# Optimization experiments

Hardware: AMD Instinct MI355X
Metric: run time of the kernel (lower is better)

## Reference

```python
import jax, jax.numpy as jnp
import numpy as np

DIM = 768
HEADS = 12
HEAD_DIM = DIM // HEADS
SCALE = DIM ** (-0.5)  # NOTE: module scales by full dim, not head_dim


def setup_inputs() -> dict:
    key = jax.random.key(0)
    k1, k2, k3 = jax.random.split(key, 3)
    B, N = 4, 2048
    x = jax.random.normal(k1, (B, N, DIM), dtype=jnp.float32)
    W_qkv = jax.random.normal(k2, (DIM, 3 * DIM), dtype=jnp.float32) * (DIM ** -0.5)
    W_proj = jax.random.normal(k3, (DIM, DIM), dtype=jnp.float32) * (DIM ** -0.5)
    b_proj = jnp.zeros((DIM,), dtype=jnp.float32)
    return {"x": x, "W_qkv": W_qkv, "W_proj": W_proj, "b_proj": b_proj}


def reference(x, W_qkv, W_proj, b_proj):
    B, N, C = x.shape
    qkv = x @ W_qkv  # [B, N, 3C]
    qkv = qkv.reshape(B, N, 3, HEADS, HEAD_DIM)
    qkv = jnp.transpose(qkv, (2, 0, 3, 1, 4))  # [3, B, H, N, hd]
    q, k, v = qkv[0], qkv[1], qkv[2]
    att = jnp.einsum('bhnd,bhmd->bhnm', q, k) * SCALE
    att = jax.nn.softmax(att, axis=-1)
    # drop=0.0 -> dropout is identity
    out = jnp.einsum('bhnm,bhmd->bhnd', att, v)  # [B, H, N, hd]
    out = jnp.transpose(out, (0, 2, 1, 3)).reshape(B, N, C)
    return out @ W_proj + b_proj
```

## Files before the change

kernel.cpp:

```cpp
#include <hip/hip_runtime.h>
#include <hip/hip_bf16.h>

#define HEADS 12
#define HD    64
#define SEQ   2048
#define CDIM  768
#define QKV_SCALE 0.03608439182435161f
#define LOG2E 1.4426950408889634f
#define SM_C (QKV_SCALE * LOG2E)

typedef __attribute__((ext_vector_type(8))) short bf16x8;
typedef __attribute__((ext_vector_type(4))) float f32x4;
typedef __attribute__((ext_vector_type(4))) unsigned short usx4;
typedef __attribute__((ext_vector_type(8))) unsigned short usx8;
typedef __attribute__((ext_vector_type(2))) unsigned int uix2;
typedef __attribute__((ext_vector_type(4))) unsigned int uix4;

__device__ __forceinline__ unsigned short f2bf(float f) {
  union { __hip_bfloat16 h; unsigned short u; } c;
  c.h = __float2bfloat16(f);
  return c.u;
}

__device__ __forceinline__ float exp2_fast(float x) {
  float r; asm("v_exp_f32 %0, %1" : "=v"(r) : "v"(x)); return r;
}

__device__ __forceinline__ unsigned int cvt_pk_bf16(float lo, float hi) {
  unsigned int r; asm("v_cvt_pk_bf16_f32 %0, %1, %2" : "=v"(r) : "v"(lo), "v"(hi)); return r;
}

__device__ __forceinline__ void gload_lds16(const unsigned short* g, unsigned short* l) {
  __builtin_amdgcn_global_load_lds(
      (__attribute__((address_space(1))) void*)(g),
      (__attribute__((address_space(3))) void*)(l), 16, 0, 0);
}

__global__ __launch_bounds__(256) void k_cvt_x(const float* __restrict__ src,
                                               unsigned short* __restrict__ dst) {
  int i = blockIdx.x * 256 + threadIdx.x;
  const float4* s4 = (const float4*)src;
  float4 a = s4[i * 2 + 0];
  float4 b = s4[i * 2 + 1];
  usx8 r;
  r[0] = f2bf(a.x); r[1] = f2bf(a.y); r[2] = f2bf(a.z); r[3] = f2bf(a.w);
  r[4] = f2bf(b.x); r[5] = f2bf(b.y); r[6] = f2bf(b.z); r[7] = f2bf(b.w);
  *(usx8*)&dst[i * 8] = r;
}

__global__ __launch_bounds__(256) void k_transpose(const float* __restrict__ src,
                                                   unsigned short* __restrict__ dst,
                                                   int K, int C) {
  __shared__ float tile[32][33];
  int tx = threadIdx.x & 31;
  int ty = threadIdx.x >> 5;
  int c0 = blockIdx.x * 32;
  int k0 = blockIdx.y * 32;
#pragma unroll
  for (int i = 0; i < 32; i += 8)
    tile[ty + i][tx] = src[(size_t)(k0 + ty + i) * C + c0 + tx];
  __syncthreads();
#pragma unroll
  for (int i = 0; i < 32; i += 8)
    dst[(size_t)(c0 + ty + i) * K + k0 + tx] = f2bf(tile[tx][ty + i]);
}

__global__ __launch_bounds__(256) void k_qkv_gemm(
    const unsigned short* __restrict__ A,
    const unsigned short* __restrict__ Bt,
    unsigned short* __restrict__ Qb, unsigned short* __restrict__ Kb,
    unsigned short* __restrict__ Vt) {
  __shared__ unsigned short As[128 * 64];
  __shared__ unsigned short Bs[128 * 64];
  const int lane = threadIdx.x & 63, w = threadIdx.x >> 6;
  const int wm = w >> 1, wn = w & 1;
  const int r0 = blockIdx.y * 128, c0 = blockIdx.x * 128;
  f32x4 acc[4][4] = {};

  for (int k0 = 0; k0 < 768; k0 += 64) {
#pragma unroll
    for (int iss = 0; iss < 4; ++iss) {
      int eo = (w * 4 + iss) * 512 + lane * 8;
      int row = eo >> 6;
      int cc = ((eo >> 3) & 7) ^ (row & 7);
      gload_lds16(A + (size_t)(r0 + row) * 768 + k0 + cc * 8, &As[(w * 4 + iss) * 512]);
    }
#pragma unroll
    for (int iss = 0; iss < 4; ++iss) {
      int eo = (w * 4 + iss) * 512 + lane * 8;
      int row = eo >> 6;
      int cc = ((eo >> 3) & 7) ^ (row & 7);
      gload_lds16(Bt + (size_t)(c0 + row) * 768 + k0 + cc * 8, &Bs[(w * 4 + iss) * 512]);
    }
    asm volatile("s_waitcnt vmcnt(0)" ::: "memory");
    __syncthreads();

#pragma unroll
    for (int ks = 0; ks < 2; ++ks) {
      bf16x8 af[4], bfr[4];
#pragma unroll
      for (int f = 0; f < 4; ++f) {
        int ar = wm * 64 + f * 16 + (lane & 15);
        int ac = (ks * 4 + (lane >> 4)) ^ (ar & 7);
        af[f] = *(const bf16x8*)&As[ar * 64 + ac * 8];
        int br = wn * 64 + f * 16 + (lane & 15);
        int bc = (ks * 4 + (lane >> 4)) ^ (br & 7);
        bfr[f] = *(const bf16x8*)&Bs[br * 64 + bc * 8];
      }
#pragma unroll
      for (int fm = 0; fm < 4; ++fm)
#pragma unroll
        for (int fn = 0; fn < 4; ++fn)
          acc[fm][fn] = __builtin_amdgcn_mfma_f32_16x16x32_bf16(af[fm], bfr[fn], acc[fm][fn], 0, 0, 0);
    }
    __syncthreads();
  }

  const int which = c0 / 768;
  const float qsc = (which == 0) ? SM_C : 1.0f;
#pragma unroll
  for (int fm = 0; fm < 4; ++fm) {
    int gr0 = r0 + wm * 64 + fm * 16 + ((lane >> 4) << 2);
    int bb = gr0 >> 11, n0 = gr0 & 2047;
#pragma unroll
    for (int fn = 0; fn < 4; ++fn) {
      int gc = c0 + wn * 64 + fn * 16 + (lane & 15);
      int rem = gc - which * 768;
      int h = rem >> 6, d = rem & 63;
      int bh = bb * HEADS + h;
      f32x4 v = acc[fm][fn];
      if (which == 2) {
        usx4 p;
        p[0] = f2bf(v[0]); p[1] = f2bf(v[1]); p[2] = f2bf(v[2]); p[3] = f2bf(v[3]);
        *(usx4*)&Vt[(size_t)(bh * 64 + d) * 2048 + n0] = p;
      } else {
        unsigned short* dst = (which == 0 ? Qb : Kb) + (size_t)(bh * 2048 + n0) * 64 + d;
        dst[0]   = f2bf(v[0] * qsc);
        dst[64]  = f2bf(v[1] * qsc);
        dst[128] = f2bf(v[2] * qsc);
        dst[192] = f2bf(v[3] * qsc);
      }
    }
  }
}

__global__ __launch_bounds__(256, 2) void k_attn(
    const unsigned short* __restrict__ Qb, const unsigned short* __restrict__ Kb,
    const unsigned short* __restrict__ Vt, unsigned short* __restrict__ Ob) {
  __shared__ unsigned short Ksm[2][64 * 64];
  __shared__ unsigned short Vsm[2][64 * 64];
  const int lane = threadIdx.x & 63, w = threadIdx.x >> 6;
  const int g = lane >> 4, c = lane & 15;

  int id = blockIdx.x + (blockIdx.y << 4);
  int lin = (id & 7) * 96 + (id >> 3);
  int bx = lin & 15, bh = lin >> 4;
  const int q0 = bx * 128 + w * 32;
  const int bb = bh / HEADS, h = bh % HEADS;

  const unsigned short* Qp = Qb + (size_t)bh * SEQ * HD;
  const unsigned short* Kp = Kb + (size_t)bh * SEQ * HD;
  const unsigned short* Vp = Vt + (size_t)bh * HD * SEQ;

  bf16x8 aQ[2][2];
#pragma unroll
  for (int qf = 0; qf < 2; ++qf)
#pragma unroll
    for (int ks = 0; ks < 2; ++ks)
      aQ[qf][ks] = *(const bf16x8*)&Qp[(size_t)(q0 + qf * 16 + c) * 64 + ks * 32 + g * 8];

  float lrun[2] = {0.f, 0.f};
  f32x4 accOT[4][2] = {};
  const f32x4 fzero = {0.f, 0.f, 0.f, 0.f};

  int offf[2][4];
#pragma unroll
  for (int ks = 0; ks < 2; ++ks)
#pragma unroll
    for (int f = 0; f < 4; ++f) {
      int row = f * 16 + c;
      offf[ks][f] = row * 64 + (((ks * 4 + g) ^ (row & 7)) * 8);
    }

  const int eo0 = (w * 2 + 0) * 512 + lane * 8;
  const int row0 = eo0 >> 6, cc0 = ((eo0 >> 3) & 7) ^ (row0 & 7);
  const int eo1 = (w * 2 + 1) * 512 + lane * 8;
  const int row1 = eo1 >> 6, cc1 = ((eo1 >> 3) & 7) ^ (row1 & 7);
  const unsigned short* kga = Kp + (size_t)row0 * 64 + cc0 * 8;
  const unsigned short* kgb = Kp + (size_t)row1 * 64 + cc1 * 8;
  const unsigned short* vga = Vp + (size_t)row0 * 2048 + cc0 * 8;
  const unsigned short* vgb = Vp + (size_t)row1 * 2048 + cc1 * 8;

  gload_lds16(kga, &Ksm[0][(w * 2 + 0) * 512]);
  gload_lds16(kgb, &Ksm[0][(w * 2 + 1) * 512]);
  gload_lds16(vga, &Vsm[0][(w * 2 + 0) * 512]);
  gload_lds16(vgb, &Vsm[0][(w * 2 + 1) * 512]);
  asm volatile("s_waitcnt vmcnt(0)" ::: "memory");
  __syncthreads();

  auto TILE = [&](int t, int buf) {
    if (t + 1 < 32) {
      gload_lds16(kga + (t + 1) * 4096, &Ksm[buf ^ 1][(w * 2 + 0) * 512]);
      gload_lds16(kgb + (t + 1) * 4096, &Ksm[buf ^ 1][(w * 2 + 1) * 512]);
      gload_lds16(vga + (t + 1) * 64,   &Vsm[buf ^ 1][(w * 2 + 0) * 512]);
      gload_lds16(vgb + (t + 1) * 64,   &Vsm[buf ^ 1][(w * 2 + 1) * 512]);
    }

    bf16x8 kf0[4], kf1[4];
#pragma unroll
    for (int fm = 0; fm < 4; ++fm) {
      kf0[fm] = *(const bf16x8*)&Ksm[buf][offf[0][fm]];
      kf1[fm] = *(const bf16x8*)&Ksm[buf][offf[1][fm]];
    }
    f32x4 st[4][2];
    __builtin_amdgcn_s_setprio(1);
#pragma unroll
    for (int fm = 0; fm < 4; ++fm)
#pragma unroll
      for (int qf = 0; qf < 2; ++qf)
        st[fm][qf] = __builtin_amdgcn_mfma_f32_16x16x32_bf16(kf0[fm], aQ[qf][0], fzero, 0, 0, 0);
#pragma unroll
    for (int fm = 0; fm < 4; ++fm)
#pragma unroll
      for (int qf = 0; qf < 2; ++qf)
        st[fm][qf] = __builtin_amdgcn_mfma_f32_16x16x32_bf16(kf1[fm], aQ[qf][1], st[fm][qf], 0, 0, 0);
    __builtin_amdgcn_s_setprio(0);

    uix4 pfrag[2][2];
#pragma unroll
    for (int qf = 0; qf < 2; ++qf) {
      float p[4][4];
      float ts[4];
#pragma unroll
      for (int fm = 0; fm < 4; ++fm) {
        p[fm][0] = exp2_fast(st[fm][qf][0]);
        p[fm][1] = exp2_fast(st[fm][qf][1]);
        p[fm][2] = exp2_fast(st[fm][qf][2]);
        p[fm][3] = exp2_fast(st[fm][qf][3]);
        ts[fm] = (p[fm][0] + p[fm][1]) + (p[fm][2] + p[fm][3]);
      }
      lrun[qf] += (ts[0] + ts[1]) + (ts[2] + ts[3]);

#pragma unroll
      for (int ks = 0; ks < 2; ++ks)
#pragma unroll
        for (int tt = 0; tt < 2; ++tt) {
          unsigned int a = cvt_pk_bf16(p[2 * ks][2 * tt], p[2 * ks][2 * tt + 1]);
          unsigned int b = cvt_pk_bf16(p[2 * ks + 1][2 * tt], p[2 * ks + 1][2 * tt + 1]);
          uix2 s1 = __builtin_amdgcn_permlane32_swap(a, b, false, false);
          uix2 s2 = __builtin_amdgcn_permlane16_swap(s1[0], s1[1], false, false);
          pfrag[ks][qf][tt] = s2[0];
          pfrag[ks][qf][2 + tt] = s2[1];
        }
    }

    bf16x8 vf0[4], vf1[4];
#pragma unroll
    for (int fd = 0; fd < 4; ++fd) {
      vf0[fd] = *(const bf16x8*)&Vsm[buf][offf[0][fd]];
      vf1[fd] = *(const bf16x8*)&Vsm[buf][offf[1][fd]];
    }
    __builtin_amdgcn_s_setprio(1);
#pragma unroll
    for (int fd = 0; fd < 4; ++fd)
#pragma unroll
      for (int qf = 0; qf < 2; ++qf) {
        accOT[fd][qf] = __builtin_amdgcn_mfma_f32_16x16x32_bf16(
            vf0[fd], *(const bf16x8*)&pfrag[0][qf], accOT[fd][qf], 0, 0, 0);
        accOT[fd][qf] = __builtin_amdgcn_mfma_f32_16x16x32_bf16(
            vf1[fd], *(const bf16x8*)&pfrag[1][qf], accOT[fd][qf], 0, 0, 0);
      }
    __builtin_amdgcn_s_setprio(0);

    asm volatile("s_waitcnt vmcnt(0)" ::: "memory");
    __syncthreads();
  };

  for (int kt = 0; kt < 32; kt += 2) {
    TILE(kt, 0);
    TILE(kt + 1, 1);
  }

#pragma unroll
  for (int qf = 0; qf < 2; ++qf) {
    float l = lrun[qf];
    l += __shfl_xor(l, 16);
    l += __shfl_xor(l, 32);
    float rl = 1.0f / l;
    int n = q0 + qf * 16 + c;
#pragma unroll
    for (int fd = 0; fd < 4; ++fd) {
      f32x4 v = accOT[fd][qf];
      usx4 pk;
      pk[0] = f2bf(v[0] * rl); pk[1] = f2bf(v[1] * rl);
      pk[2] = f2bf(v[2] * rl); pk[3] = f2bf(v[3] * rl);
      *(usx4*)&Ob[(size_t)(bb * SEQ + n) * CDIM + h * HD + fd * 16 + 4 * g] = pk;
    }
  }
}

__global__ __launch_bounds__(256) void k_proj_gemm(
    const unsigned short* __restrict__ A,
    const unsigned short* __restrict__ Bt,
    const float* __restrict__ bias, float* __restrict__ out) {
  __shared__ unsigned short As[128 * 64];
  __shared__ unsigned short Bs[128 * 64];
  const int lane = threadIdx.x & 63, w = threadIdx.x >> 6;
  const int wm = w >> 1, wn = w & 1;
  const int r0 = blockIdx.y * 128, c0 = blockIdx.x * 128;
  f32x4 acc[4][4] = {};

  for (int k0 = 0; k0 < 768; k0 += 64) {
#pragma unroll
    for (int iss = 0; iss < 4; ++iss) {
      int eo = (w * 4 + iss) * 512 + lane * 8;
      int row = eo >> 6;
      int cc = ((eo >> 3) & 7) ^ (row & 7);
      gload_lds16(A + (size_t)(r0 + row) * 768 + k0 + cc * 8, &As[(w * 4 + iss) * 512]);
    }
#pragma unroll
    for (int iss = 0; iss < 4; ++iss) {
      int eo = (w * 4 + iss) * 512 + lane * 8;
      int row = eo >> 6;
      int cc = ((eo >> 3) & 7) ^ (row & 7);
      gload_lds16(Bt + (size_t)(c0 + row) * 768 + k0 + cc * 8, &Bs[(w * 4 + iss) * 512]);
    }
    asm volatile("s_waitcnt vmcnt(0)" ::: "memory");
    __syncthreads();

#pragma unroll
    for (int ks = 0; ks < 2; ++ks) {
      bf16x8 af[4], bfr[4];
#pragma unroll
      for (int f = 0; f < 4; ++f) {
        int ar = wm * 64 + f * 16 + (lane & 15);
        int ac = (ks * 4 + (lane >> 4)) ^ (ar & 7);
        af[f] = *(const bf16x8*)&As[ar * 64 + ac * 8];
        int br = wn * 64 + f * 16 + (lane & 15);
        int bc = (ks * 4 + (lane >> 4)) ^ (br & 7);
        bfr[f] = *(const bf16x8*)&Bs[br * 64 + bc * 8];
      }
#pragma unroll
      for (int fm = 0; fm < 4; ++fm)
#pragma unroll
        for (int fn = 0; fn < 4; ++fn)
          acc[fm][fn] = __builtin_amdgcn_mfma_f32_16x16x32_bf16(af[fm], bfr[fn], acc[fm][fn], 0, 0, 0);
    }
    __syncthreads();
  }

#pragma unroll
  for (int fm = 0; fm < 4; ++fm) {
    int gr0 = r0 + wm * 64 + fm * 16 + ((lane >> 4) << 2);
#pragma unroll
    for (int fn = 0; fn < 4; ++fn) {
      int gc = c0 + wn * 64 + fn * 16 + (lane & 15);
      float bsv = bias[gc];
      f32x4 v = acc[fm][fn];
#pragma unroll
      for (int r = 0; r < 4; ++r)
        out[(size_t)(gr0 + r) * CDIM + gc] = v[r] + bsv;
    }
  }
}

extern "C" void kernel_launch(void* const* d_in, const int* in_sizes, int n_in,
                              void* d_out, int out_size, void* d_ws, size_t ws_size,
                              hipStream_t stream) {
  const float* x      = (const float*)d_in[0];
  const float* W_qkv  = (const float*)d_in[1];
  const float* W_proj = (const float*)d_in[2];
  const float* b_proj = (const float*)d_in[3];
  float* out = (float*)d_out;

  unsigned short* ws     = (unsigned short*)d_ws;
  unsigned short* xb     = ws;
  unsigned short* WqkvT  = xb + 6291456;
  unsigned short* WprojT = WqkvT + 1769472;
  unsigned short* Qb     = WprojT + 589824;
  unsigned short* Kb     = Qb + 6291456;
  unsigned short* Vt     = Kb + 6291456;
  unsigned short* Ob     = Vt + 6291456;

  k_cvt_x<<<3072, 256, 0, stream>>>(x, xb);
  k_transpose<<<dim3(72, 24), 256, 0, stream>>>(W_qkv, WqkvT, 768, 2304);
  k_transpose<<<dim3(24, 24), 256, 0, stream>>>(W_proj, WprojT, 768, 768);
  k_qkv_gemm<<<dim3(18, 64), 256, 0, stream>>>(xb, WqkvT, Qb, Kb, Vt);
  k_attn<<<dim3(16, 48), 256, 0, stream>>>(Qb, Kb, Vt, Ob);
  k_proj_gemm<<<dim3(6, 64), 256, 0, stream>>>(Ob, WprojT, b_proj, out);
}
```

Baseline: 144.6 us.

## Merge prep kernels, remap GEMM blocks for XCD locality, shrink proj tile

Folds the x conversion and both weight transposes into one launch, which removes two kernel launches. Remaps the block index in both GEMMs so that consecutive blocks land on the same XCD, aiming for better L2 reuse. Halves the proj GEMM M tile to 64, doubling the grid to 768 blocks so the 256 CUs are filled better, at the cost of less reuse per block.

Result: faster. 136.8 us (-5.4%).

```diff
diff --git a/kernel.cpp b/kernel.cpp
--- a/kernel.cpp
+++ b/kernel.cpp
@@ -36,33 +36,42 @@
       (__attribute__((address_space(3))) void*)(l), 16, 0, 0);
 }
 
-__global__ __launch_bounds__(256) void k_cvt_x(const float* __restrict__ src,
-                                               unsigned short* __restrict__ dst) {
-  int i = blockIdx.x * 256 + threadIdx.x;
-  const float4* s4 = (const float4*)src;
-  float4 a = s4[i * 2 + 0];
-  float4 b = s4[i * 2 + 1];
-  usx8 r;
-  r[0] = f2bf(a.x); r[1] = f2bf(a.y); r[2] = f2bf(a.z); r[3] = f2bf(a.w);
-  r[4] = f2bf(b.x); r[5] = f2bf(b.y); r[6] = f2bf(b.z); r[7] = f2bf(b.w);
-  *(usx8*)&dst[i * 8] = r;
-}
-
-__global__ __launch_bounds__(256) void k_transpose(const float* __restrict__ src,
-                                                   unsigned short* __restrict__ dst,
-                                                   int K, int C) {
+__global__ __launch_bounds__(256) void k_prep(
+    const float* __restrict__ x, unsigned short* __restrict__ xb,
+    const float* __restrict__ Wqkv, unsigned short* __restrict__ WqkvT,
+    const float* __restrict__ Wproj, unsigned short* __restrict__ WprojT) {
   __shared__ float tile[32][33];
+  const int b = blockIdx.x;
+  if (b < 3072) {
+    int i = b * 256 + threadIdx.x;
+    const float4* s4 = (const float4*)x;
+    float4 a = s4[i * 2 + 0];
+    float4 d = s4[i * 2 + 1];
+    usx8 r;
+    r[0] = f2bf(a.x); r[1] = f2bf(a.y); r[2] = f2bf(a.z); r[3] = f2bf(a.w);
+    r[4] = f2bf(d.x); r[5] = f2bf(d.y); r[6] = f2bf(d.z); r[7] = f2bf(d.w);
+    *(usx8*)&xb[i * 8] = r;
+    return;
+  }
+  const float* src; unsigned short* dst; int C, c0, k0;
+  if (b < 4800) {
+    int tb = b - 3072;
+    src = Wqkv; dst = WqkvT; C = 2304;
+    c0 = (tb % 72) * 32; k0 = (tb / 72) * 32;
+  } else {
+    int tb = b - 4800;
+    src = Wproj; dst = WprojT; C = 768;
+    c0 = (tb % 24) * 32; k0 = (tb / 24) * 32;
+  }
   int tx = threadIdx.x & 31;
   int ty = threadIdx.x >> 5;
-  int c0 = blockIdx.x * 32;
-  int k0 = blockIdx.y * 32;
 #pragma unroll
   for (int i = 0; i < 32; i += 8)
     tile[ty + i][tx] = src[(size_t)(k0 + ty + i) * C + c0 + tx];
   __syncthreads();
 #pragma unroll
   for (int i = 0; i < 32; i += 8)
-    dst[(size_t)(c0 + ty + i) * K + k0 + tx] = f2bf(tile[tx][ty + i]);
+    dst[(size_t)(c0 + ty + i) * 768 + k0 + tx] = f2bf(tile[tx][ty + i]);
 }
 
 __global__ __launch_bounds__(256) void k_qkv_gemm(
@@ -74,7 +83,9 @@
   __shared__ unsigned short Bs[128 * 64];
   const int lane = threadIdx.x & 63, w = threadIdx.x >> 6;
   const int wm = w >> 1, wn = w & 1;
-  const int r0 = blockIdx.y * 128, c0 = blockIdx.x * 128;
+  const int id = blockIdx.y * 18 + blockIdx.x;
+  const int lin = (id & 7) * 144 + (id >> 3);
+  const int r0 = (lin / 18) * 128, c0 = (lin % 18) * 128;
   f32x4 acc[4][4] = {};
 
   for (int k0 = 0; k0 < 768; k0 += 64) {
@@ -303,20 +314,22 @@
     const unsigned short* __restrict__ A,
     const unsigned short* __restrict__ Bt,
     const float* __restrict__ bias, float* __restrict__ out) {
-  __shared__ unsigned short As[128 * 64];
+  __shared__ unsigned short As[64 * 64];
   __shared__ unsigned short Bs[128 * 64];
   const int lane = threadIdx.x & 63, w = threadIdx.x >> 6;
-  const int wm = w >> 1, wn = w & 1;
-  const int r0 = blockIdx.y * 128, c0 = blockIdx.x * 128;
-  f32x4 acc[4][4] = {};
+  const int wm = w & 1, wn = w >> 1;
+  const int id = blockIdx.y * 6 + blockIdx.x;
+  const int lin = (id & 7) * 96 + (id >> 3);
+  const int r0 = (lin / 6) * 64, c0 = (lin % 6) * 128;
+  f32x4 acc[2][4] = {};
 
   for (int k0 = 0; k0 < 768; k0 += 64) {
 #pragma unroll
-    for (int iss = 0; iss < 4; ++iss) {
-      int eo = (w * 4 + iss) * 512 + lane * 8;
+    for (int iss = 0; iss < 2; ++iss) {
+      int eo = (w * 2 + iss) * 512 + lane * 8;
       int row = eo >> 6;
       int cc = ((eo >> 3) & 7) ^ (row & 7);
-      gload_lds16(A + (size_t)(r0 + row) * 768 + k0 + cc * 8, &As[(w * 4 + iss) * 512]);
+      gload_lds16(A + (size_t)(r0 + row) * 768 + k0 + cc * 8, &As[(w * 2 + iss) * 512]);
     }
 #pragma unroll
     for (int iss = 0; iss < 4; ++iss) {
@@ -330,18 +343,21 @@
 
 #pragma unroll
     for (int ks = 0; ks < 2; ++ks) {
-      bf16x8 af[4], bfr[4];
-#pragma unroll
-      for (int f = 0; f < 4; ++f) {
-        int ar = wm * 64 + f * 16 + (lane & 15);
+      bf16x8 af[2], bfr[4];
+#pragma unroll
+      for (int f = 0; f < 2; ++f) {
+        int ar = wm * 32 + f * 16 + (lane & 15);
         int ac = (ks * 4 + (lane >> 4)) ^ (ar & 7);
         af[f] = *(const bf16x8*)&As[ar * 64 + ac * 8];
+      }
+#pragma unroll
+      for (int f = 0; f < 4; ++f) {
         int br = wn * 64 + f * 16 + (lane & 15);
         int bc = (ks * 4 + (lane >> 4)) ^ (br & 7);
         bfr[f] = *(const bf16x8*)&Bs[br * 64 + bc * 8];
       }
 #pragma unroll
-      for (int fm = 0; fm < 4; ++fm)
+      for (int fm = 0; fm < 2; ++fm)
 #pragma unroll
         for (int fn = 0; fn < 4; ++fn)
           acc[fm][fn] = __builtin_amdgcn_mfma_f32_16x16x32_bf16(af[fm], bfr[fn], acc[fm][fn], 0, 0, 0);
@@ -350,8 +366,8 @@
   }
 
 #pragma unroll
-  for (int fm = 0; fm < 4; ++fm) {
-    int gr0 = r0 + wm * 64 + fm * 16 + ((lane >> 4) << 2);
+  for (int fm = 0; fm < 2; ++fm) {
+    int gr0 = r0 + wm * 32 + fm * 16 + ((lane >> 4) << 2);
 #pragma unroll
     for (int fn = 0; fn < 4; ++fn) {
       int gc = c0 + wn * 64 + fn * 16 + (lane & 15);
@@ -382,10 +398,8 @@
   unsigned short* Vt     = Kb + 6291456;
   unsigned short* Ob     = Vt + 6291456;
 
-  k_cvt_x<<<3072, 256, 0, stream>>>(x, xb);
-  k_transpose<<<dim3(72, 24), 256, 0, stream>>>(W_qkv, WqkvT, 768, 2304);
-  k_transpose<<<dim3(24, 24), 256, 0, stream>>>(W_proj, WprojT, 768, 768);
+  k_prep<<<5376, 256, 0, stream>>>(x, xb, W_qkv, WqkvT, W_proj, WprojT);
   k_qkv_gemm<<<dim3(18, 64), 256, 0, stream>>>(xb, WqkvT, Qb, Kb, Vt);
   k_attn<<<dim3(16, 48), 256, 0, stream>>>(Qb, Kb, Vt, Ob);
-  k_proj_gemm<<<dim3(6, 64), 256, 0, stream>>>(Ob, WprojT, b_proj, out);
-}
+  k_proj_gemm<<<dim3(6, 128), 256, 0, stream>>>(Ob, WprojT, b_proj, out);
+}
```
